# Performance work log

Hardware: AMD Instinct MI355X
Metric: run time of the kernel (lower is better)

Reference implementation:

```python
import jax, jax.numpy as jnp
import numpy as np

N, T, D_FEAT, H = 8192, 60, 6, 64
NEG_SLOPE = 0.01  # torch LeakyReLU default


def setup_inputs() -> dict:
    key = jax.random.key(0)
    ks = jax.random.split(key, 20)
    s = lambda k, shape, fan: jax.random.normal(k, shape, jnp.float32) * (1.0 / np.sqrt(fan))
    inp = {
        'x': jax.random.normal(ks[0], (N, T, D_FEAT), jnp.float32),
        # LSTM layer 0 (input D_FEAT) and layer 1 (input H); gate order i,f,g,o
        'Wih0': s(ks[1], (4 * H, D_FEAT), H), 'Whh0': s(ks[2], (4 * H, H), H),
        'bih0': s(ks[3], (4 * H,), H), 'bhh0': s(ks[4], (4 * H,), H),
        'Wih1': s(ks[5], (4 * H, H), H), 'Whh1': s(ks[6], (4 * H, H), H),
        'bih1': s(ks[7], (4 * H,), H), 'bhh1': s(ks[8], (4 * H,), H),
        # GAT layer: transformation Linear(H,H) and attention vector a [2H,1] (randn in torch)
        'Wt': s(ks[9], (H, H), H), 'bt': s(ks[10], (H,), H),
        'a': jax.random.normal(ks[11], (2 * H, 1), jnp.float32),
        # fc and fc_out
        'Wfc': s(ks[12], (H, H), H), 'bfc': s(ks[13], (H,), H),
        'Wout': s(ks[14], (1, H), H), 'bout': s(ks[15], (1,), H),
    }
    return inp


def _lstm_layer(x, Wih, Whh, bih, bhh):
    # x: [N, T, Din] -> outputs [N, T, H]
    xg = jnp.einsum('ntd,gd->ntg', x, Wih) + bih + bhh  # precompute input gates

    def step(carry, xt):
        h, c = carry
        gates = xt + h @ Whh.T  # [N, 4H]
        i, f, g, o = jnp.split(gates, 4, axis=-1)
        c = jax.nn.sigmoid(f) * c + jax.nn.sigmoid(i) * jnp.tanh(g)
        h = jax.nn.sigmoid(o) * jnp.tanh(c)
        return (h, c), h

    n = x.shape[0]
    h0 = jnp.zeros((n, Whh.shape[1]), x.dtype)
    (_, _), hs = jax.lax.scan(step, (h0, h0), jnp.swapaxes(xg, 0, 1))
    return jnp.swapaxes(hs, 0, 1)


def _gat_layer(x, Wt, bt, a):
    # att[i,j] = leaky_relu(a1 . Wx_j + a2 . Wx_i); softmax over j; out = att @ x
    h = x @ Wt.T + bt                    # [N, H]
    hdim = h.shape[1]
    s1 = (h @ a[:hdim]).squeeze(-1)      # a1 . Wx_j  -> column term
    s2 = (h @ a[hdim:]).squeeze(-1)      # a2 . Wx_i  -> row term
    scores = jax.nn.leaky_relu(s2[:, None] + s1[None, :], NEG_SLOPE)  # [N, N]
    att = jax.nn.softmax(scores, axis=1)
    return att @ x


def reference(x, Wih0, Whh0, bih0, bhh0, Wih1, Whh1, bih1, bhh1,
              Wt, bt, a, Wfc, bfc, Wout, bout):
    out = _lstm_layer(x, Wih0, Whh0, bih0, bhh0)
    out = _lstm_layer(out, Wih1, Whh1, bih1, bhh1)
    last = out[:, -1, :]                 # [N, H]
    hidden = _gat_layer(last, Wt, bt, a) + last  # num_layers_gat = 1
    hidden = jax.nn.leaky_relu(hidden @ Wfc.T + bfc, NEG_SLOPE)
    return (hidden @ Wout.T + bout).squeeze(-1)  # [N]
```

## Files before the change

kernel.cpp:

```cpp
#include <hip/hip_runtime.h>

#define NN 8192
#define TT 60
#define DF 6
#define HH 64
#define GG 256
#define RS 132
#define CH 32
#define NB 256

typedef _Float16 half8 __attribute__((ext_vector_type(8)));
typedef float f32x4 __attribute__((ext_vector_type(4)));
#define MFMA16(a, b, c) __builtin_amdgcn_mfma_f32_16x16x32_f16((a), (b), (c), 0, 0, 0)

__device__ __forceinline__ float sigmoidf_(float x) {
    return __builtin_amdgcn_rcpf(1.0f + __expf(-x));
}
__device__ __forceinline__ float tanhf_(float x) {
    return __builtin_fmaf(2.0f, __builtin_amdgcn_rcpf(1.0f + __expf(-2.0f * x)), -1.0f);
}
__device__ __forceinline__ float lrelu_(float x) { return x > 0.0f ? x : 0.01f * x; }

__device__ __forceinline__ half8 ldw8(const float* __restrict__ p) {
    const float4* q = (const float4*)p;
    float4 u = q[0], v = q[1];
    half8 r;
    r[0]=(_Float16)u.x; r[1]=(_Float16)u.y; r[2]=(_Float16)u.z; r[3]=(_Float16)u.w;
    r[4]=(_Float16)v.x; r[5]=(_Float16)v.y; r[6]=(_Float16)v.z; r[7]=(_Float16)v.w;
    return r;
}

#define SXW (TT * 8 + 8)

__global__ __launch_bounds__(512, 4)
void lstm_fused_kernel(const float* __restrict__ x,
                       const float* __restrict__ Wih0, const float* __restrict__ Whh0,
                       const float* __restrict__ bih0, const float* __restrict__ bhh0,
                       const float* __restrict__ Wih1, const float* __restrict__ Whh1,
                       const float* __restrict__ bih1, const float* __restrict__ bhh1,
                       const float* __restrict__ Wt, const float* __restrict__ bt,
                       const float* __restrict__ av,
                       float* __restrict__ last_out,
                       float* __restrict__ s1g, float* __restrict__ s2g)
{
    __shared__ _Float16 sxp[16][SXW];
    __shared__ _Float16 h0buf[2][16][72];
    __shared__ _Float16 h1buf[2][16][72];
    __shared__ _Float16 zero16[8];
    __shared__ float sv1[HH], sv2[HH], sc12[2];

    const int tid  = threadIdx.x;
    const int w    = tid >> 6;
    const int grp  = w >> 2;
    const int cg   = w & 3;
    const int lane = tid & 63;
    const int quad = lane >> 4;
    const int l15  = lane & 15;
    const int hc   = cg * 16 + l15;
    const int n0   = blockIdx.x * 16;

    for (int i = tid; i < 16 * SXW / 2; i += 512) ((unsigned*)sxp)[i] = 0u;
    for (int i = tid; i < 2 * 16 * 72 / 2; i += 512) ((unsigned*)h0buf)[i] = 0u;
    for (int i = tid; i < 2 * 16 * 72 / 2; i += 512) ((unsigned*)h1buf)[i] = 0u;
    if (tid < 4) ((unsigned*)zero16)[tid] = 0u;
    __syncthreads();

    for (int idx = tid; idx < 16 * TT * DF; idx += 512) {
        const int m = idx / (TT * DF);
        const int r = idx - m * (TT * DF);
        const int t = r / DF;
        const int d = r - t * DF;
        sxp[m][t * 8 + d] = (_Float16)x[(size_t)(n0 + m) * (TT * DF) + r];
    }

    if (tid < HH) {
        float a1 = 0.f, a2 = 0.f;
        #pragma unroll 8
        for (int h = 0; h < HH; h++) {
            const float wt = Wt[h * HH + tid];
            a1 += wt * av[h];
            a2 += wt * av[HH + h];
        }
        sv1[tid] = a1; sv2[tid] = a2;
    } else if (tid == 64 || tid == 65) {
        const float* ap = av + (tid - 64) * HH;
        float c = 0.f;
        #pragma unroll 8
        for (int h = 0; h < HH; h++) c += bt[h] * ap[h];
        sc12[tid - 64] = c;
    }

    half8 wA[4][2], wB[4][2];
    float bias[4];
    half8 hzero;
    #pragma unroll
    for (int j = 0; j < 8; j++) hzero[j] = (_Float16)0.f;

    if (grp == 0) {
        #pragma unroll
        for (int nt = 0; nt < 4; nt++) {
            const int g = nt * 64 + hc;
            wA[nt][0] = ldw8(Whh0 + (size_t)g * HH + quad * 8);
            wA[nt][1] = ldw8(Whh0 + (size_t)g * HH + 32 + quad * 8);
            bias[nt]  = bih0[g] + bhh0[g];
            half8 t = hzero;
            if (quad == 0) {
                #pragma unroll
                for (int j = 0; j < DF; j++) t[j] = (_Float16)Wih0[g * DF + j];
            }
            wB[nt][0] = t;
            wB[nt][1] = hzero;
        }
    } else {
        #pragma unroll
        for (int nt = 0; nt < 4; nt++) {
            const int g = nt * 64 + hc;
            wA[nt][0] = ldw8(Wih1 + (size_t)g * HH + quad * 8);
            wA[nt][1] = ldw8(Wih1 + (size_t)g * HH + 32 + quad * 8);
            wB[nt][0] = ldw8(Whh1 + (size_t)g * HH + quad * 8);
            wB[nt][1] = ldw8(Whh1 + (size_t)g * HH + 32 + quad * 8);
            bias[nt]  = bih1[g] + bhh1[g];
        }
    }

    float cs[4] = {0.f, 0.f, 0.f, 0.f};
    __syncthreads();

    for (int i = 0; i <= TT; i++) {
        const int p = i & 1;
        if (grp == 0) {
            if (i < TT) {
                const half8 a0 = *(const half8*)&h0buf[p][l15][quad * 8];
                const half8 a1 = *(const half8*)&h0buf[p][l15][32 + quad * 8];
                const _Float16* xap = (quad == 0) ? &sxp[l15][i * 8] : zero16;
                const half8 ax = *(const half8*)xap;
                f32x4 gv[4];
                #pragma unroll
                for (int nt = 0; nt < 4; nt++) {
                    f32x4 c; c[0] = bias[nt]; c[1] = bias[nt]; c[2] = bias[nt]; c[3] = bias[nt];
                    c = MFMA16(ax, wB[nt][0], c);
                    c = MFMA16(a0, wA[nt][0], c);
                    c = MFMA16(a1, wA[nt][1], c);
                    gv[nt] = c;
                }
                _Float16 (*h0w)[72] = h0buf[p ^ 1];
                #pragma unroll
                for (int reg = 0; reg < 4; reg++) {
                    const float gi = gv[0][reg], gf = gv[1][reg], gc = gv[2][reg], go = gv[3][reg];
                    const float cc = sigmoidf_(gf) * cs[reg] + sigmoidf_(gi) * tanhf_(gc);
                    cs[reg] = cc;
                    h0w[quad * 4 + reg][hc] = (_Float16)(sigmoidf_(go) * tanhf_(cc));
                }
            }
        } else {
            if (i > 0) {
                const half8 a00 = *(const half8*)&h0buf[p][l15][quad * 8];
                const half8 a01 = *(const half8*)&h0buf[p][l15][32 + quad * 8];
                const half8 a10 = *(const half8*)&h1buf[p][l15][quad * 8];
                const half8 a11 = *(const half8*)&h1buf[p][l15][32 + quad * 8];
                f32x4 gv[4];
                #pragma unroll
                for (int nt = 0; nt < 4; nt++) {
                    f32x4 c; c[0] = bias[nt]; c[1] = bias[nt]; c[2] = bias[nt]; c[3] = bias[nt];
                    c = MFMA16(a00, wA[nt][0], c);
                    c = MFMA16(a01, wA[nt][1], c);
                    c = MFMA16(a10, wB[nt][0], c);
                    c = MFMA16(a11, wB[nt][1], c);
                    gv[nt] = c;
                }
                _Float16 (*h1w)[72] = h1buf[p ^ 1];
                #pragma unroll
                for (int reg = 0; reg < 4; reg++) {
                    const float gi = gv[0][reg], gf = gv[1][reg], gc = gv[2][reg], go = gv[3][reg];
                    const float cc = sigmoidf_(gf) * cs[reg] + sigmoidf_(gi) * tanhf_(gc);
                    cs[reg] = cc;
                    const float hv = sigmoidf_(go) * tanhf_(cc);
                    h1w[quad * 4 + reg][hc] = (_Float16)hv;
                    if (i == TT) last_out[(size_t)(n0 + quad * 4 + reg) * HH + hc] = hv;
                }
            }
        }
        __syncthreads();
    }

    {
        const _Float16 (*hf)[72] = h1buf[1];
        const int r  = tid >> 5;
        const int c0 = tid & 31;
        const float h1a = (float)hf[r][c0];
        const float h1b = (float)hf[r][c0 + 32];
        float p1 = h1a * sv1[c0] + h1b * sv1[c0 + 32];
        float p2 = h1a * sv2[c0] + h1b * sv2[c0 + 32];
        #pragma unroll
        for (int off = 16; off > 0; off >>= 1) {
            p1 += __shfl_xor(p1, off);
            p2 += __shfl_xor(p2, off);
        }
        if (c0 == 0) {
            s1g[n0 + r] = p1 + sc12[0];
            s2g[n0 + r] = p2 + sc12[1];
        }
    }
}

__global__ __launch_bounds__(256)
void rankfac_kernel(const float* __restrict__ s1g, const float* __restrict__ s2g,
                    float* __restrict__ Z, float* __restrict__ Ai, float* __restrict__ Bi,
                    float* __restrict__ U, float* __restrict__ W,
                    int* __restrict__ iperm, float* __restrict__ sortedD)
{
    __shared__ float sb[NN];
    __shared__ float sred[256];
    __shared__ int   sRank[32];
    const int tid = threadIdx.x;
    const int b   = blockIdx.x;
    const int j0  = b * 32;

    for (int idx = tid; idx < NN; idx += 256) sb[idx] = s1g[idx];
    if (tid < 32) sRank[tid] = 0;
    __syncthreads();

    float m = -1e30f;
    for (int idx = tid; idx < NN; idx += 256) m = fmaxf(m, sb[idx]);
    sred[tid] = m;
    __syncthreads();
    for (int s = 128; s > 0; s >>= 1) {
        if (tid < s) sred[tid] = fmaxf(sred[tid], sred[tid + s]);
        __syncthreads();
    }
    const float s1max = sred[0];

    if (tid < 32) {
        const int j = j0 + tid;
        const float z  = s2g[j] + s1max;
        const float mi = lrelu_(z);
        Z[j]  = z;
        Ai[j] = __expf(z - mi);
        Bi[j] = __expf(0.01f * z - mi);
        const float d = sb[j] - s1max;
        U[j] = __expf(d);
        W[j] = __expf(0.01f * d);
    }
    {
        const int jl = tid & 31;
        const int part = tid >> 5;
        const float sj = sb[j0 + jl];
        const int jg = j0 + jl;
        int cnt = 0;
        const int k0 = part * (NN / 8);
        #pragma unroll 4
        for (int k = k0; k < k0 + NN / 8; k++) {
            const float sk = sb[k];
            cnt += (sk < sj || (sk == sj && k < jg)) ? 1 : 0;
        }
        atomicAdd(&sRank[jl], cnt);
    }
    __syncthreads();
    if (tid < 32) {
        const int r = sRank[tid];
        iperm[r] = j0 + tid;
        sortedD[r] = sb[j0 + tid] - s1max;
    }
}

__global__ __launch_bounds__(256)
void scanA_kernel(const float* __restrict__ last, const float* __restrict__ U,
                  const float* __restrict__ W, const int* __restrict__ iperm,
                  float* __restrict__ chunkSum)
{
    __shared__ int   sj[CH];
    __shared__ float su[CH], sw[CH];
    __shared__ float al[CH][HH], bl[CH][HH];
    const int tid = threadIdx.x;
    const int b   = blockIdx.x;
    if (tid < CH) {
        const int j = iperm[b * CH + tid];
        sj[tid] = j; su[tid] = U[j]; sw[tid] = W[j];
    }
    __syncthreads();
    for (int idx = tid; idx < CH * HH; idx += 256) {
        const int rr = idx >> 6, c = idx & 63;
        const float lv = last[(size_t)sj[rr] * HH + c];
        al[rr][c] = su[rr] * lv;
        bl[rr][c] = sw[rr] * lv;
    }
    __syncthreads();
    if (tid < 130) {
        const int c = tid;
        float s = 0.f;
        if (c < 64) {
            for (int rr = 0; rr < CH; rr++) s += al[rr][c];
        } else if (c < 128) {
            for (int rr = 0; rr < CH; rr++) s += bl[rr][c - 64];
        } else if (c == 128) {
            for (int rr = 0; rr < CH; rr++) s += su[rr];
        } else {
            for (int rr = 0; rr < CH; rr++) s += sw[rr];
        }
        chunkSum[b * RS + c] = s;
    }
}

__global__ __launch_bounds__(256)
void scanB_kernel(const float* __restrict__ chunkSum, float* __restrict__ chunkOfs)
{
    __shared__ float wt[4];
    const int c   = blockIdx.x;
    const bool rev = (c < 64) || (c == 128);
    const int tid = threadIdx.x;
    const int lane = tid & 63, wv = tid >> 6;
    const int idx = rev ? (NB - 1 - tid) : tid;
    const float orig = chunkSum[idx * RS + c];
    float v = orig;
    #pragma unroll
    for (int d = 1; d < 64; d <<= 1) {
        const float t = __shfl_up(v, d);
        if (lane >= d) v += t;
    }
    if (lane == 63) wt[wv] = v;
    __syncthreads();
    float off = 0.f;
    for (int q = 0; q < wv; q++) off += wt[q];
    chunkOfs[idx * RS + c] = v + off - orig;
}

__global__ __launch_bounds__(256)
void scanC_kernel(const float* __restrict__ last, const float* __restrict__ U,
                  const float* __restrict__ W, const int* __restrict__ iperm,
                  const float* __restrict__ chunkOfs, float* __restrict__ PP)
{
    __shared__ int   sj[CH];
    __shared__ float su[CH], sw[CH];
    __shared__ float al[CH][HH], bl[CH][HH];
    const int tid = threadIdx.x;
    const int b   = blockIdx.x;
    if (tid < CH) {
        const int j = iperm[b * CH + tid];
        sj[tid] = j; su[tid] = U[j]; sw[tid] = W[j];
    }
    __syncthreads();
    for (int idx = tid; idx < CH * HH; idx += 256) {
        const int rr = idx >> 6, c = idx & 63;
        const float lv = last[(size_t)sj[rr] * HH + c];
        al[rr][c] = su[rr] * lv;
        bl[rr][c] = sw[rr] * lv;
    }
    __syncthreads();
    if (tid < 130) {
        const int c = tid;
        const bool rev = (c < 64) || (c == 128);
        float run = chunkOfs[b * RS + c];
        if (rev) {
            if (b == NB - 1) PP[(size_t)NN * RS + c] = 0.f;
            for (int rr = CH - 1; rr >= 0; rr--) {
                const float val = (c < 64) ? al[rr][c] : su[rr];
                run += val;
                PP[(size_t)(b * CH + rr) * RS + c] = run;
            }
        } else {
            for (int rr = 0; rr < CH; rr++) {
                PP[(size_t)(b * CH + rr) * RS + c] = run;
                run += (c < 128) ? bl[rr][c - 64] : sw[rr];
            }
            if (b == NB - 1) PP[(size_t)NN * RS + c] = run;
        }
    }
}

__global__ __launch_bounds__(256)
void applyfc_kernel(const float* __restrict__ last,
                    const float* __restrict__ Z, const float* __restrict__ Ai, const float* __restrict__ Bi,
                    const float* __restrict__ sortedD, const float* __restrict__ PP,
                    const float* __restrict__ Wfc, const float* __restrict__ bfc,
                    const float* __restrict__ Wout, const float* __restrict__ bout,
                    float* __restrict__ out)
{
    __shared__ float sdD[NN];
    __shared__ float sW[HH][HH + 1];
    __shared__ float sbF[HH], saF[HH];
    const int tid = threadIdx.x;
    for (int idx = tid; idx < NN; idx += 256) sdD[idx] = sortedD[idx];
    for (int idx = tid; idx < HH * HH; idx += 256) {
        const int h = idx >> 6, d = idx & 63;
        sW[d][h] = Wfc[idx];
    }
    if (tid < HH) { sbF[tid] = bfc[tid]; saF[tid] = Wout[tid]; }
    __syncthreads();

    const int wv = tid >> 6, lane = tid & 63;
    const int i0 = blockIdx.x * 32 + wv * 8;
    float zi[8]; int lo[8], hi[8];
    #pragma unroll
    for (int q = 0; q < 8; q++) { zi[q] = Z[i0 + q]; lo[q] = 0; hi[q] = NN; }
    for (int iter = 0; iter < 13; iter++) {
        #pragma unroll
        for (int q = 0; q < 8; q++) {
            if (lo[q] < hi[q]) {
                const int mid = (lo[q] + hi[q]) >> 1;
                const float dm = sdD[mid];
                if (zi[q] + dm > 0.f) hi[q] = mid; else lo[q] = mid + 1;
            }
        }
    }
    float gv[8];
    #pragma unroll
    for (int q = 0; q < 8; q++) {
        const int i = i0 + q;
        const float* rowp = PP + (size_t)lo[q] * RS;
        const float pu  = rowp[lane];
        const float pw  = rowp[64 + lane];
        const float pud = rowp[128];
        const float pwd = rowp[129];
        const float ai = Ai[i], bi = Bi[i];
        const float numer = bi * pw + ai * pu;
        const float den   = bi * pwd + ai * pud;
        const float lv = last[(size_t)i * HH + lane];
        gv[q] = numer * __builtin_amdgcn_rcpf(den) + lv;
    }
    const float bo = bout[0];
    #pragma unroll
    for (int q = 0; q < 8; q++) {
        float acc = sbF[lane];
        #pragma unroll
        for (int d = 0; d < HH; d++) acc += __shfl(gv[q], d) * sW[d][lane];
        float prod = lrelu_(acc) * saF[lane];
        #pragma unroll
        for (int off = 32; off > 0; off >>= 1) prod += __shfl_xor(prod, off);
        if (lane == 0) out[i0 + q] = prod + bo;
    }
}

extern "C" void kernel_launch(void* const* d_in, const int* in_sizes, int n_in,
                              void* d_out, int out_size, void* d_ws, size_t ws_size,
                              hipStream_t stream)
{
    (void)in_sizes; (void)n_in; (void)out_size; (void)ws_size;
    const float* x    = (const float*)d_in[0];
    const float* Wih0 = (const float*)d_in[1];
    const float* Whh0 = (const float*)d_in[2];
    const float* bih0 = (const float*)d_in[3];
    const float* bhh0 = (const float*)d_in[4];
    const float* Wih1 = (const float*)d_in[5];
    const float* Whh1 = (const float*)d_in[6];
    const float* bih1 = (const float*)d_in[7];
    const float* bhh1 = (const float*)d_in[8];
    const float* Wt   = (const float*)d_in[9];
    const float* bt   = (const float*)d_in[10];
    const float* a    = (const float*)d_in[11];
    const float* Wfc  = (const float*)d_in[12];
    const float* bfc  = (const float*)d_in[13];
    const float* Wout = (const float*)d_in[14];
    const float* bout = (const float*)d_in[15];
    float* out = (float*)d_out;

    float* ws       = (float*)d_ws;
    float* last     = ws;
    float* s1g      = last + (size_t)NN*HH;
    float* s2g      = s1g + NN;
    float* Z        = s2g + NN;
    float* Ai       = Z + NN;
    float* Bi       = Ai + NN;
    float* U        = Bi + NN;
    float* W        = U + NN;
    float* sortedD  = W + NN;
    int*   iperm    = (int*)(sortedD + NN);
    float* chunkSum = (float*)(iperm + NN);
    float* chunkOfs = chunkSum + NB*RS;
    float* PP       = chunkOfs + NB*RS;

    lstm_fused_kernel<<<dim3(NN / 16), dim3(512), 0, stream>>>(
        x, Wih0, Whh0, bih0, bhh0, Wih1, Whh1, bih1, bhh1,
        Wt, bt, a, last, s1g, s2g);
    rankfac_kernel<<<dim3(NB), dim3(256), 0, stream>>>(
        s1g, s2g, Z, Ai, Bi, U, W, iperm, sortedD);
    scanA_kernel<<<dim3(NB), dim3(256), 0, stream>>>(last, U, W, iperm, chunkSum);
    scanB_kernel<<<dim3(130), dim3(256), 0, stream>>>(chunkSum, chunkOfs);
    scanC_kernel<<<dim3(NB), dim3(256), 0, stream>>>(last, U, W, iperm, chunkOfs, PP);
    applyfc_kernel<<<dim3(NB), dim3(256), 0, stream>>>(
        last, Z, Ai, Bi, sortedD, PP, Wfc, bfc, Wout, bout, out);
}
```

Measured before the change: 260.3 us.

## Fuse chunk-sum scan into rank kernel via atomic scatter, drop scan kernels

Chunk sums over the sorted order are now built by the rank kernel, which atomically adds each row's weighted vectors into its destination chunk. The LSTM kernel zeroes the chunk-sum buffer, and the PP fill kernel computes each chunk's offset by summing all other chunks directly instead of using a separate scan kernel. This removes two kernel launches and a gather pass. In exchange it adds float atomics, which make the summation order nondeterministic, and a redundant 256-element loop per column in every block.

```diff
diff --git a/kernel.cpp b/kernel.cpp
--- a/kernel.cpp
+++ b/kernel.cpp
@@ -41,7 +41,8 @@
                        const float* __restrict__ Wt, const float* __restrict__ bt,
                        const float* __restrict__ av,
                        float* __restrict__ last_out,
-                       float* __restrict__ s1g, float* __restrict__ s2g)
+                       float* __restrict__ s1g, float* __restrict__ s2g,
+                       float* __restrict__ chunkSum)
 {
     __shared__ _Float16 sxp[16][SXW];
     __shared__ _Float16 h0buf[2][16][72];
@@ -58,6 +59,11 @@
     const int l15  = lane & 15;
     const int hc   = cg * 16 + l15;
     const int n0   = blockIdx.x * 16;
+
+    {
+        const int base = blockIdx.x * 66;
+        for (int q = tid; q < 66; q += 512) chunkSum[base + q] = 0.f;
+    }
 
     for (int i = tid; i < 16 * SXW / 2; i += 512) ((unsigned*)sxp)[i] = 0u;
     for (int i = tid; i < 2 * 16 * 72 / 2; i += 512) ((unsigned*)h0buf)[i] = 0u;
@@ -204,14 +210,17 @@
 }
 
 __global__ __launch_bounds__(256)
-void rankfac_kernel(const float* __restrict__ s1g, const float* __restrict__ s2g,
-                    float* __restrict__ Z, float* __restrict__ Ai, float* __restrict__ Bi,
-                    float* __restrict__ U, float* __restrict__ W,
-                    int* __restrict__ iperm, float* __restrict__ sortedD)
+void rankscatter_kernel(const float* __restrict__ s1g, const float* __restrict__ s2g,
+                        const float* __restrict__ last,
+                        float* __restrict__ Z, float* __restrict__ Ai, float* __restrict__ Bi,
+                        float* __restrict__ U, float* __restrict__ W,
+                        int* __restrict__ iperm, float* __restrict__ sortedD,
+                        float* __restrict__ chunkSum)
 {
     __shared__ float sb[NN];
     __shared__ float sred[256];
     __shared__ int   sRank[32];
+    __shared__ float sU[32], sWw[32];
     const int tid = threadIdx.x;
     const int b   = blockIdx.x;
     const int j0  = b * 32;
@@ -238,9 +247,12 @@
         Ai[j] = __expf(z - mi);
         Bi[j] = __expf(0.01f * z - mi);
         const float d = sb[j] - s1max;
-        U[j] = __expf(d);
-        W[j] = __expf(0.01f * d);
-    }
+        const float u = __expf(d);
+        const float ww = __expf(0.01f * d);
+        U[j] = u; W[j] = ww;
+        sU[tid] = u; sWw[tid] = ww;
+    }
+    __syncthreads();
     {
         const int jl = tid & 31;
         const int part = tid >> 5;
@@ -261,12 +273,29 @@
         iperm[r] = j0 + tid;
         sortedD[r] = sb[j0 + tid] - s1max;
     }
+    __syncthreads();
+    const int wv = tid >> 6, lane = tid & 63;
+    #pragma unroll
+    for (int jj = 0; jj < 8; jj++) {
+        const int jl = wv * 8 + jj;
+        const int j  = j0 + jl;
+        const int c  = sRank[jl] >> 5;
+        const float u = sU[jl], ww = sWw[jl];
+        const float lv = last[(size_t)j * HH + lane];
+        float* dst = chunkSum + (size_t)c * RS;
+        atomicAdd(&dst[lane],      u * lv);
+        atomicAdd(&dst[64 + lane], ww * lv);
+        if (lane == 0) {
+            atomicAdd(&dst[128], u);
+            atomicAdd(&dst[129], ww);
+        }
+    }
 }
 
 __global__ __launch_bounds__(256)
-void scanA_kernel(const float* __restrict__ last, const float* __restrict__ U,
-                  const float* __restrict__ W, const int* __restrict__ iperm,
-                  float* __restrict__ chunkSum)
+void ppfill_kernel(const float* __restrict__ last, const float* __restrict__ U,
+                   const float* __restrict__ W, const int* __restrict__ iperm,
+                   const float* __restrict__ chunkSum, float* __restrict__ PP)
 {
     __shared__ int   sj[CH];
     __shared__ float su[CH], sw[CH];
@@ -287,69 +316,12 @@
     __syncthreads();
     if (tid < 130) {
         const int c = tid;
-        float s = 0.f;
-        if (c < 64) {
-            for (int rr = 0; rr < CH; rr++) s += al[rr][c];
-        } else if (c < 128) {
-            for (int rr = 0; rr < CH; rr++) s += bl[rr][c - 64];
-        } else if (c == 128) {
-            for (int rr = 0; rr < CH; rr++) s += su[rr];
-        } else {
-            for (int rr = 0; rr < CH; rr++) s += sw[rr];
-        }
-        chunkSum[b * RS + c] = s;
-    }
-}
-
-__global__ __launch_bounds__(256)
-void scanB_kernel(const float* __restrict__ chunkSum, float* __restrict__ chunkOfs)
-{
-    __shared__ float wt[4];
-    const int c   = blockIdx.x;
-    const bool rev = (c < 64) || (c == 128);
-    const int tid = threadIdx.x;
-    const int lane = tid & 63, wv = tid >> 6;
-    const int idx = rev ? (NB - 1 - tid) : tid;
-    const float orig = chunkSum[idx * RS + c];
-    float v = orig;
-    #pragma unroll
-    for (int d = 1; d < 64; d <<= 1) {
-        const float t = __shfl_up(v, d);
-        if (lane >= d) v += t;
-    }
-    if (lane == 63) wt[wv] = v;
-    __syncthreads();
-    float off = 0.f;
-    for (int q = 0; q < wv; q++) off += wt[q];
-    chunkOfs[idx * RS + c] = v + off - orig;
-}
-
-__global__ __launch_bounds__(256)
-void scanC_kernel(const float* __restrict__ last, const float* __restrict__ U,
-                  const float* __restrict__ W, const int* __restrict__ iperm,
-                  const float* __restrict__ chunkOfs, float* __restrict__ PP)
-{
-    __shared__ int   sj[CH];
-    __shared__ float su[CH], sw[CH];
-    __shared__ float al[CH][HH], bl[CH][HH];
-    const int tid = threadIdx.x;
-    const int b   = blockIdx.x;
-    if (tid < CH) {
-        const int j = iperm[b * CH + tid];
-        sj[tid] = j; su[tid] = U[j]; sw[tid] = W[j];
-    }
-    __syncthreads();
-    for (int idx = tid; idx < CH * HH; idx += 256) {
-        const int rr = idx >> 6, c = idx & 63;
-        const float lv = last[(size_t)sj[rr] * HH + c];
-        al[rr][c] = su[rr] * lv;
-        bl[rr][c] = sw[rr] * lv;
-    }
-    __syncthreads();
-    if (tid < 130) {
-        const int c = tid;
         const bool rev = (c < 64) || (c == 128);
-        float run = chunkOfs[b * RS + c];
+        float run = 0.f;
+        for (int bb = 0; bb < NB; bb++) {
+            const float v = chunkSum[bb * RS + c];
+            run += ((rev ? (bb > b) : (bb < b)) ? v : 0.f);
+        }
         if (rev) {
             if (b == NB - 1) PP[(size_t)NN * RS + c] = 0.f;
             for (int rr = CH - 1; rr >= 0; rr--) {
@@ -465,17 +437,15 @@
     float* sortedD  = W + NN;
     int*   iperm    = (int*)(sortedD + NN);
     float* chunkSum = (float*)(iperm + NN);
-    float* chunkOfs = chunkSum + NB*RS;
-    float* PP       = chunkOfs + NB*RS;
+    float* PP       = chunkSum + NB*RS;
 
     lstm_fused_kernel<<<dim3(NN / 16), dim3(512), 0, stream>>>(
         x, Wih0, Whh0, bih0, bhh0, Wih1, Whh1, bih1, bhh1,
-        Wt, bt, a, last, s1g, s2g);
-    rankfac_kernel<<<dim3(NB), dim3(256), 0, stream>>>(
-        s1g, s2g, Z, Ai, Bi, U, W, iperm, sortedD);
-    scanA_kernel<<<dim3(NB), dim3(256), 0, stream>>>(last, U, W, iperm, chunkSum);
-    scanB_kernel<<<dim3(130), dim3(256), 0, stream>>>(chunkSum, chunkOfs);
-    scanC_kernel<<<dim3(NB), dim3(256), 0, stream>>>(last, U, W, iperm, chunkOfs, PP);
+        Wt, bt, a, last, s1g, s2g, chunkSum);
+    rankscatter_kernel<<<dim3(NB), dim3(256), 0, stream>>>(
+        s1g, s2g, last, Z, Ai, Bi, U, W, iperm, sortedD, chunkSum);
+    ppfill_kernel<<<dim3(NB), dim3(256), 0, stream>>>(
+        last, U, W, iperm, chunkSum, PP);
     applyfc_kernel<<<dim3(NB), dim3(256), 0, stream>>>(
         last, Z, Ai, Bi, sortedD, PP, Wfc, bfc, Wout, bout, out);
 }
```

Result: slower. 294.4 us (+13.1%).
